# Kernel optimization log

Hardware: AMD Instinct MI355X
Metric: run time of the kernel (lower is better)

Reference implementation:

```python
import jax, jax.numpy as jnp
import numpy as np

B, H, W, C = 16, 64, 64, 512
NH, WS, SS = 16, 8, 4
HD = C // NH
N = WS * WS
MLP = 4 * C
EPS = 1e-5


def window_partition(x, ws):
    b, h, w, c = x.shape
    x = x.reshape(b, h // ws, ws, w // ws, ws, c).transpose(0, 1, 3, 2, 4, 5)
    return x.reshape(-1, ws, ws, c)


def window_reverse(win, ws, h, w):
    c = win.shape[-1]
    x = win.reshape(-1, h // ws, w // ws, ws, ws, c).transpose(0, 1, 3, 2, 4, 5)
    return x.reshape(-1, h, w, c)


def _rel_pos_index():
    coords = np.stack(np.meshgrid(np.arange(WS), np.arange(WS), indexing='ij'))  # [2,WS,WS]
    cf = coords.reshape(2, -1)
    rc = (cf[:, :, None] - cf[:, None, :]).transpose(1, 2, 0)  # [N,N,2]
    rc[:, :, 0] += WS - 1
    rc[:, :, 1] += WS - 1
    rc[:, :, 0] *= 2 * WS - 1
    return jnp.asarray(rc.sum(-1), dtype=jnp.int32)  # [N,N]


def _attn_mask():
    # region ids for shifted windows (HF get_attn_mask)
    img = np.zeros((1, H, W, 1), dtype=np.float32)
    slices = (slice(0, -WS), slice(-WS, -SS), slice(-SS, None))
    cnt = 0
    for hs in slices:
        for ws_ in slices:
            img[:, hs, ws_, :] = cnt
            cnt += 1
    mw = np.asarray(window_partition(jnp.asarray(img), WS)).reshape(-1, N)  # [nw,N]
    mask = mw[:, None, :] - mw[:, :, None]
    mask = np.where(mask != 0, -100.0, 0.0).astype(np.float32)
    return jnp.asarray(mask)  # [nw,N,N]


REL_IDX = _rel_pos_index()
ATTN_MASK = _attn_mask()


def layer_norm(x, g, b):
    mu = x.mean(-1, keepdims=True)
    var = ((x - mu) ** 2).mean(-1, keepdims=True)
    return (x - mu) * jax.lax.rsqrt(var + EPS) * g + b


def setup_inputs() -> dict:
    key = jax.random.key(0)
    ks = jax.random.split(key, 16)
    s = 0.02
    return {
        'hidden_states': jax.random.normal(ks[0], (B, H * W, C), jnp.float32),
        'q_w': jax.random.normal(ks[1], (C, C), jnp.float32) * s,
        'q_b': jnp.zeros((C,), jnp.float32),
        'k_w': jax.random.normal(ks[2], (C, C), jnp.float32) * s,
        'k_b': jnp.zeros((C,), jnp.float32),
        'v_w': jax.random.normal(ks[3], (C, C), jnp.float32) * s,
        'v_b': jnp.zeros((C,), jnp.float32),
        'proj_w': jax.random.normal(ks[4], (C, C), jnp.float32) * s,
        'proj_b': jnp.zeros((C,), jnp.float32),
        'rel_bias_table': jax.random.normal(ks[5], ((2 * WS - 1) * (2 * WS - 1), NH), jnp.float32) * s,
        'ln1_w': jnp.ones((C,), jnp.float32),
        'ln1_b': jnp.zeros((C,), jnp.float32),
        'ln2_w': jnp.ones((C,), jnp.float32),
        'ln2_b': jnp.zeros((C,), jnp.float32),
        'fc1_w': jax.random.normal(ks[6], (MLP, C), jnp.float32) * s,
        'fc1_b': jnp.zeros((MLP,), jnp.float32),
        'fc2_w': jax.random.normal(ks[7], (C, MLP), jnp.float32) * s,
        'fc2_b': jnp.zeros((C,), jnp.float32),
    }


def reference(hidden_states, q_w, q_b, k_w, k_b, v_w, v_b, proj_w, proj_b,
              rel_bias_table, ln1_w, ln1_b, ln2_w, ln2_b, fc1_w, fc1_b, fc2_w, fc2_b):
    shortcut = hidden_states
    x = layer_norm(hidden_states, ln1_w, ln1_b).reshape(B, H, W, C)
    # cyclic shift
    x = jnp.roll(x, (-SS, -SS), axis=(1, 2))
    win = window_partition(x, WS).reshape(-1, N, C)  # [B*nw, N, C]
    Bw = win.shape[0]

    def heads(t):  # [Bw,N,C] -> [Bw,NH,N,HD]
        return t.reshape(Bw, N, NH, HD).transpose(0, 2, 1, 3)

    q = heads(win @ q_w.T + q_b)
    k = heads(win @ k_w.T + k_b)
    v = heads(win @ v_w.T + v_b)

    scores = jnp.einsum('bhnd,bhmd->bhnm', q, k) / jnp.sqrt(jnp.float32(HD))
    bias = rel_bias_table[REL_IDX.reshape(-1)].reshape(N, N, NH).transpose(2, 0, 1)  # [NH,N,N]
    scores = scores + bias[None]
    nw = ATTN_MASK.shape[0]
    scores = scores.reshape(Bw // nw, nw, NH, N, N) + ATTN_MASK[None, :, None]
    scores = scores.reshape(Bw, NH, N, N)
    probs = jax.nn.softmax(scores, axis=-1)
    ctx = jnp.einsum('bhnm,bhmd->bhnd', probs, v).transpose(0, 2, 1, 3).reshape(Bw, N, C)
    attn_out = ctx @ proj_w.T + proj_b

    shifted = window_reverse(attn_out.reshape(-1, WS, WS, C), WS, H, W)
    x = jnp.roll(shifted, (SS, SS), axis=(1, 2)).reshape(B, H * W, C)
    h = shortcut + x

    y = layer_norm(h, ln2_w, ln2_b)
    y = jax.nn.gelu(y @ fc1_w.T + fc1_b, approximate=False)
    y = y @ fc2_w.T + fc2_b
    return h + y
```

## Files before the change

kernel.cpp:

```cpp
#include <hip/hip_runtime.h>
#include <cmath>
#include <cstdint>
#include <cstddef>

typedef __bf16 bf16;
typedef __bf16 bf16x8 __attribute__((ext_vector_type(8)));
typedef float f32x4 __attribute__((ext_vector_type(4)));

#define DEVINL __device__ __forceinline__

DEVINL void gload_lds16(const bf16* g, bf16* l) {
    __builtin_amdgcn_global_load_lds(
        (const __attribute__((address_space(1))) void*)g,
        (__attribute__((address_space(3))) void*)l,
        16, 0, 0);
}

DEVINL bool probe_f32(const uint32_t* probe) { return *probe == 0x3F800000u; }

#define OFF_QW  0u
#define OFF_KW  262144u
#define OFF_VW  524288u
#define OFF_PW  786432u
#define OFF_F1W 1048576u
#define OFF_F2W 2097152u
#define OFF_REL 3145728u
#define OFF_QB  3149328u
#define OFF_KB  3149840u
#define OFF_VB  3150352u
#define OFF_PB  3150864u
#define OFF_L1W 3151376u
#define OFF_L1B 3151888u
#define OFF_L2W 3152400u
#define OFF_L2B 3152912u
#define OFF_F1B 3153424u
#define OFF_F2B 3155472u
#define PRM_TOT 3155984u

struct P17 { const void* p[17]; };

__global__ __launch_bounds__(256) void conv_params(P17 ps, const uint32_t* probe,
                                                   bf16* __restrict__ dst) {
    const size_t off[18] = {OFF_QW, OFF_KW, OFF_VW, OFF_PW, OFF_F1W, OFF_F2W,
                            OFF_REL, OFF_QB, OFF_KB, OFF_VB, OFF_PB, OFF_L1W,
                            OFF_L1B, OFF_L2W, OFF_L2B, OFF_F1B, OFF_F2B, PRM_TOT};
    size_t e = ((size_t)blockIdx.x * 256 + threadIdx.x) * 8;
    if (e >= PRM_TOT) return;
    int s = 0;
#pragma unroll
    for (int i = 1; i < 17; ++i) s = (e >= off[i]) ? i : s;
    const size_t loc = e - off[s];
    if (probe_f32(probe)) {
        const float* sp = (const float*)ps.p[s] + loc;
        bf16x8 o;
#pragma unroll
        for (int t = 0; t < 8; ++t) o[t] = (bf16)sp[t];
        *(bf16x8*)(dst + e) = o;
    } else {
        *(bf16x8*)(dst + e) = *(const bf16x8*)((const bf16*)ps.p[s] + loc);
    }
}

__global__ __launch_bounds__(256) void conv_hidden(const void* __restrict__ src,
                                                   const uint32_t* probe,
                                                   bf16* __restrict__ dst,
                                                   size_t base_elt) {
    size_t e = ((size_t)blockIdx.x * 256 + threadIdx.x) * 8;
    if (probe_f32(probe)) {
        const float* sp = (const float*)src + base_elt + e;
        bf16x8 o;
#pragma unroll
        for (int t = 0; t < 8; ++t) o[t] = (bf16)sp[t];
        *(bf16x8*)(dst + e) = o;
    } else {
        *(bf16x8*)(dst + e) = *(const bf16x8*)((const bf16*)src + base_elt + e);
    }
}

template <int MODE>
__global__ __launch_bounds__(256) void ln_kernel(const bf16* __restrict__ srcb,
                                                 const float* __restrict__ srcf,
                                                 const bf16* __restrict__ g,
                                                 const bf16* __restrict__ bb,
                                                 bf16* __restrict__ out) {
    const int row = blockIdx.x * 4 + (threadIdx.x >> 6);
    const int lane = threadIdx.x & 63;
    size_t srow;
    if (MODE == 0) {
        int win = row >> 6, t = row & 63;
        int b = win >> 6, wi = win & 63;
        int hs = ((wi >> 3) << 3) + (t >> 3);
        int ws = ((wi & 7) << 3) + (t & 7);
        srow = (size_t)b * 4096 + (size_t)((hs + 4) & 63) * 64 + ((ws + 4) & 63);
    } else {
        srow = row;
    }
    float x[8];
    if (MODE == 0) {
        bf16x8 vv = *(const bf16x8*)(srcb + srow * 512 + lane * 8);
#pragma unroll
        for (int t = 0; t < 8; ++t) x[t] = (float)vv[t];
    } else {
        const f32x4* p = (const f32x4*)(srcf + srow * 512 + lane * 8);
        f32x4 a = p[0], c = p[1];
#pragma unroll
        for (int t = 0; t < 4; ++t) { x[t] = a[t]; x[4 + t] = c[t]; }
    }
    float s = 0.f, s2 = 0.f;
#pragma unroll
    for (int t = 0; t < 8; ++t) { s += x[t]; s2 += x[t] * x[t]; }
    for (int off = 1; off < 64; off <<= 1) {
        s += __shfl_xor(s, off, 64);
        s2 += __shfl_xor(s2, off, 64);
    }
    const float mu = s * (1.0f / 512.0f);
    const float var = s2 * (1.0f / 512.0f) - mu * mu;
    const float rs = rsqrtf(var + 1e-5f);
    bf16x8 gg = *(const bf16x8*)(g + lane * 8);
    bf16x8 bv = *(const bf16x8*)(bb + lane * 8);
    bf16x8 o;
#pragma unroll
    for (int t = 0; t < 8; ++t)
        o[t] = (bf16)(((x[t] - mu) * rs) * (float)gg[t] + (float)bv[t]);
    *(bf16x8*)(out + (size_t)row * 512 + lane * 8) = o;
}

template <int N, int K, int EPI>
__global__ __launch_bounds__(256) void gemm_bt(const bf16* __restrict__ A,
                                               const bf16* __restrict__ W,
                                               const bf16* __restrict__ bias,
                                               void* __restrict__ outp,
                                               const bf16* __restrict__ auxb,
                                               const float* __restrict__ auxf,
                                               size_t obase,
                                               const uint32_t* probe) {
    __shared__ bf16 sA[128 * 32];
    __shared__ bf16 sB[128 * 32];
    const int tid = threadIdx.x;
    const int bm = blockIdx.x, bn = blockIdx.y;
    const int wave = tid >> 6, lane = tid & 63;
    const int wm = (wave >> 1) << 6, wn = (wave & 1) << 6;
    const int lrow = lane & 15, quad = lane >> 4;

    bool f32o = false;
    if constexpr (EPI == 3) f32o = probe_f32(probe);

    f32x4 acc[4][4] = {};
    const bf16* Ab = A + (size_t)bm * 128 * K;
    const bf16* Wb = W + (size_t)bn * 128 * K;

    const int e0 = tid * 8;
    const int e1 = (256 + tid) * 8;
    const int r0 = e0 >> 5, c0 = e0 & 31;
    const int r1 = e1 >> 5, c1 = e1 & 31;

    for (int k0 = 0; k0 < K; k0 += 32) {
        gload_lds16(Ab + (size_t)r0 * K + k0 + c0, &sA[e0]);
        gload_lds16(Ab + (size_t)r1 * K + k0 + c1, &sA[e1]);
        gload_lds16(Wb + (size_t)r0 * K + k0 + c0, &sB[e0]);
        gload_lds16(Wb + (size_t)r1 * K + k0 + c1, &sB[e1]);
        __syncthreads();
        bf16x8 af[4], bfr[4];
#pragma unroll
        for (int i = 0; i < 4; ++i)
            af[i] = *(const bf16x8*)&sA[(wm + i * 16 + lrow) * 32 + quad * 8];
#pragma unroll
        for (int j = 0; j < 4; ++j)
            bfr[j] = *(const bf16x8*)&sB[(wn + j * 16 + lrow) * 32 + quad * 8];
#pragma unroll
        for (int i = 0; i < 4; ++i)
#pragma unroll
            for (int j = 0; j < 4; ++j)
                acc[i][j] = __builtin_amdgcn_mfma_f32_16x16x32_bf16(af[i], bfr[j], acc[i][j], 0, 0, 0);
        __syncthreads();
    }

#pragma unroll
    for (int i = 0; i < 4; ++i) {
#pragma unroll
        for (int r = 0; r < 4; ++r) {
            const int m = bm * 128 + wm + i * 16 + quad * 4 + r;
            size_t dest = 0;
            if (EPI == 1) {
                int win = m >> 6, t = m & 63;
                int b = win >> 6, wi = win & 63;
                int hs = ((wi >> 3) << 3) + (t >> 3);
                int ws = ((wi & 7) << 3) + (t & 7);
                dest = (size_t)b * 4096 + (size_t)((hs + 4) & 63) * 64 + ((ws + 4) & 63);
            }
#pragma unroll
            for (int j = 0; j < 4; ++j) {
                const int n = bn * 128 + wn + j * 16 + lrow;
                float v = acc[i][j][r] + (float)bias[n];
                if (EPI == 0) {
                    ((bf16*)outp)[(size_t)m * N + n] = (bf16)v;
                } else if (EPI == 1) {
                    ((float*)outp)[dest * 512 + n] = v + (float)auxb[dest * 512 + n];
                } else if (EPI == 2) {
                    float gl = 0.5f * v * (1.0f + erff(v * 0.70710678118654752f));
                    ((bf16*)outp)[(size_t)m * N + n] = (bf16)gl;
                } else {
                    float o = v + auxf[(size_t)m * N + n];
                    if (f32o) ((float*)outp)[obase + (size_t)m * N + n] = o;
                    else      ((bf16*)outp)[obase + (size_t)m * N + n] = (bf16)o;
                }
            }
        }
    }
}

__global__ __launch_bounds__(256) void attn_kernel(const bf16* __restrict__ q,
                                                   const bf16* __restrict__ k,
                                                   const bf16* __restrict__ v,
                                                   const bf16* __restrict__ table,
                                                   bf16* __restrict__ ctx) {
    __shared__ bf16 sVt[4][32 * 64];
    __shared__ bf16 sP[4][64 * 64];
    const int win = blockIdx.x;
    const int wave = threadIdx.x >> 6, lane = threadIdx.x & 63;
    const int head = blockIdx.y * 4 + wave;
    const int lrow = lane & 15, quad = lane >> 4;
    const size_t base = (size_t)win * 64 * 512 + head * 32;

    {
        const bf16* vr = v + base + (size_t)lane * 512;
#pragma unroll
        for (int d0 = 0; d0 < 32; d0 += 8) {
            bf16x8 vv = *(const bf16x8*)(vr + d0);
#pragma unroll
            for (int t = 0; t < 8; ++t) sVt[wave][(d0 + t) * 64 + lane] = vv[t];
        }
    }

    f32x4 sacc[4][4] = {};
    {
        bf16x8 qa[4], kb[4];
#pragma unroll
        for (int i = 0; i < 4; ++i)
            qa[i] = *(const bf16x8*)(q + base + (size_t)(i * 16 + lrow) * 512 + quad * 8);
#pragma unroll
        for (int j = 0; j < 4; ++j)
            kb[j] = *(const bf16x8*)(k + base + (size_t)(j * 16 + lrow) * 512 + quad * 8);
#pragma unroll
        for (int i = 0; i < 4; ++i)
#pragma unroll
            for (int j = 0; j < 4; ++j)
                sacc[i][j] = __builtin_amdgcn_mfma_f32_16x16x32_bf16(qa[i], kb[j], sacc[i][j], 0, 0, 0);
    }

    const int wi = win & 63;
    const int hb8 = (wi >> 3) << 3, wb8 = (wi & 7) << 3;
    const float scale = 0.17677669529663689f;
#pragma unroll
    for (int ti = 0; ti < 4; ++ti) {
#pragma unroll
        for (int r = 0; r < 4; ++r) {
            const int i = ti * 16 + quad * 4 + r;
            const int ih = i >> 3, iw = i & 7;
            const int ah = hb8 + ih, aw = wb8 + iw;
            const int rgi = ((ah < 56) ? 0 : (ah < 60) ? 1 : 2) * 3 +
                            ((aw < 56) ? 0 : (aw < 60) ? 1 : 2);
            float rowmax = -1e30f;
#pragma unroll
            for (int tj = 0; tj < 4; ++tj) {
                const int j = tj * 16 + lrow;
                const int jh = j >> 3, jw = j & 7;
                const int bh = hb8 + jh, bw = wb8 + jw;
                const int rgj = ((bh < 56) ? 0 : (bh < 60) ? 1 : 2) * 3 +
                                ((bw < 56) ? 0 : (bw < 60) ? 1 : 2);
                const int ridx = (ih - jh + 7) * 15 + (iw - jw + 7);
                float sv = sacc[ti][tj][r] * scale + (float)table[ridx * 16 + head] +
                           ((rgi == rgj) ? 0.0f : -100.0f);
                sacc[ti][tj][r] = sv;
                rowmax = fmaxf(rowmax, sv);
            }
            for (int off = 1; off < 16; off <<= 1)
                rowmax = fmaxf(rowmax, __shfl_xor(rowmax, off, 64));
            float rsum = 0.f;
#pragma unroll
            for (int tj = 0; tj < 4; ++tj) {
                float e = __expf(sacc[ti][tj][r] - rowmax);
                sacc[ti][tj][r] = e;
                rsum += e;
            }
            for (int off = 1; off < 16; off <<= 1) rsum += __shfl_xor(rsum, off, 64);
            const float inv = 1.0f / rsum;
#pragma unroll
            for (int tj = 0; tj < 4; ++tj)
                sP[wave][(size_t)i * 64 + tj * 16 + lrow] = (bf16)(sacc[ti][tj][r] * inv);
        }
    }
    __syncthreads();

    f32x4 cacc[4][2] = {};
#pragma unroll
    for (int ks = 0; ks < 2; ++ks) {
        bf16x8 vbf[2];
#pragma unroll
        for (int tn = 0; tn < 2; ++tn)
            vbf[tn] = *(const bf16x8*)&sVt[wave][(tn * 16 + lrow) * 64 + ks * 32 + quad * 8];
#pragma unroll
        for (int mi = 0; mi < 4; ++mi) {
            bf16x8 pa = *(const bf16x8*)&sP[wave][(size_t)(mi * 16 + lrow) * 64 + ks * 32 + quad * 8];
#pragma unroll
            for (int tn = 0; tn < 2; ++tn)
                cacc[mi][tn] = __builtin_amdgcn_mfma_f32_16x16x32_bf16(pa, vbf[tn], cacc[mi][tn], 0, 0, 0);
        }
    }
#pragma unroll
    for (int mi = 0; mi < 4; ++mi)
#pragma unroll
        for (int tn = 0; tn < 2; ++tn)
#pragma unroll
            for (int r = 0; r < 4; ++r) {
                const int i = mi * 16 + quad * 4 + r;
                const int d = tn * 16 + lrow;
                ctx[base + (size_t)i * 512 + d] = (bf16)cacc[mi][tn][r];
            }
}

extern "C" void kernel_launch(void* const* d_in, const int* in_sizes, int n_in,
                              void* d_out, int out_size, void* d_ws, size_t ws_size,
                              hipStream_t stream) {
    (void)in_sizes; (void)n_in; (void)out_size;
    const uint32_t* probe = (const uint32_t*)d_in[10];
    char* ws = (char*)d_ws;
    const size_t MB = (size_t)1 << 20;

    bf16* prm = (bf16*)ws;
    P17 ps;
    ps.p[0] = d_in[1];  ps.p[1] = d_in[3];  ps.p[2] = d_in[5];  ps.p[3] = d_in[7];
    ps.p[4] = d_in[14]; ps.p[5] = d_in[16]; ps.p[6] = d_in[9];  ps.p[7] = d_in[2];
    ps.p[8] = d_in[4];  ps.p[9] = d_in[6];  ps.p[10] = d_in[8]; ps.p[11] = d_in[10];
    ps.p[12] = d_in[11]; ps.p[13] = d_in[12]; ps.p[14] = d_in[13];
    ps.p[15] = d_in[15]; ps.p[16] = d_in[17];
    conv_params<<<dim3((PRM_TOT / 8 + 255) / 256), dim3(256), 0, stream>>>(ps, probe, prm);

    int nb = 1;
    for (int c = 16; c >= 2; c >>= 1)
        if (8 * MB + (size_t)c * 36 * MB <= ws_size) { nb = c; break; }
    const size_t R = (size_t)nb * 4096;
    char* arena = ws + 8 * MB;
    bf16* hidC = (bf16*)(arena);
    bf16* Xc   = (bf16*)(arena + 1024 * R);
    bf16* qc   = (bf16*)(arena + 2048 * R);
    bf16* kc   = (bf16*)(arena + 3072 * R);
    bf16* vc   = (bf16*)(arena + 4096 * R);
    float* hc  = (float*)(arena + 5120 * R);
    bf16* a1   = (bf16*)(arena + 7168 * R);

    const int nchunks = 16 / nb;
    const size_t Mh = R / 2;

    for (int cb = 0; cb < nchunks; ++cb) {
        conv_hidden<<<dim3((unsigned)(R / 4)), dim3(256), 0, stream>>>(
            d_in[0], probe, hidC, (size_t)cb * R * 512);

        ln_kernel<0><<<dim3((unsigned)(R / 4)), dim3(256), 0, stream>>>(
            hidC, nullptr, prm + OFF_L1W, prm + OFF_L1B, Xc);

        gemm_bt<512, 512, 0><<<dim3((unsigned)(R / 128), 4), dim3(256), 0, stream>>>(
            Xc, prm + OFF_QW, prm + OFF_QB, qc, nullptr, nullptr, 0, nullptr);
        gemm_bt<512, 512, 0><<<dim3((unsigned)(R / 128), 4), dim3(256), 0, stream>>>(
            Xc, prm + OFF_KW, prm + OFF_KB, kc, nullptr, nullptr, 0, nullptr);
        gemm_bt<512, 512, 0><<<dim3((unsigned)(R / 128), 4), dim3(256), 0, stream>>>(
            Xc, prm + OFF_VW, prm + OFF_VB, vc, nullptr, nullptr, 0, nullptr);

        attn_kernel<<<dim3((unsigned)(R / 64), 4), dim3(256), 0, stream>>>(
            qc, kc, vc, prm + OFF_REL, Xc);

        gemm_bt<512, 512, 1><<<dim3((unsigned)(R / 128), 4), dim3(256), 0, stream>>>(
            Xc, prm + OFF_PW, prm + OFF_PB, hc, hidC, nullptr, 0, nullptr);

        ln_kernel<1><<<dim3((unsigned)(R / 4)), dim3(256), 0, stream>>>(
            nullptr, hc, prm + OFF_L2W, prm + OFF_L2B, Xc);

        for (int hf = 0; hf < 2; ++hf) {
            gemm_bt<2048, 512, 2><<<dim3((unsigned)(Mh / 128), 16), dim3(256), 0, stream>>>(
                Xc + (size_t)hf * Mh * 512, prm + OFF_F1W, prm + OFF_F1B, a1,
                nullptr, nullptr, 0, nullptr);
            gemm_bt<512, 2048, 3><<<dim3((unsigned)(Mh / 128), 4), dim3(256), 0, stream>>>(
                a1, prm + OFF_F2W, prm + OFF_F2B, d_out,
                nullptr, hc + (size_t)hf * Mh * 512,
                ((size_t)cb * R + (size_t)hf * Mh) * 512, probe);
        }
    }
}
```

Baseline: 1.271 ms.

## Rewrite GEMM as 256x256-tile, 8-wave, double-buffered swizzled LDS pipeline

Result: slower. 1.978 ms (+55.7%).

```diff
diff --git a/kernel.cpp b/kernel.cpp
--- a/kernel.cpp
+++ b/kernel.cpp
@@ -125,8 +125,115 @@
     *(bf16x8*)(out + (size_t)row * 512 + lane * 8) = o;
 }
 
+
+template <int K>
+DEVINL void stage_two(const bf16* src, char* reg, int k0, int tid, int sswz,
+                      int X0, int X1) {
+    {
+        const int X = X0 + tid * 16;
+        const int sx = X ^ sswz;
+        gload_lds16(src + (size_t)(sx >> 7) * K + (k0 + ((sx & 127) >> 1)),
+                    (bf16*)(reg + X));
+    }
+    {
+        const int X = X1 + tid * 16;
+        const int sx = X ^ sswz;
+        gload_lds16(src + (size_t)(sx >> 7) * K + (k0 + ((sx & 127) >> 1)),
+                    (bf16*)(reg + X));
+    }
+}
+
+template <int K, int PART>
+DEVINL void stage_part(const bf16* Ab, const bf16* Wb, char* lds, int tile,
+                       int tid, int sswz) {
+    constexpr bool isB = (PART == 1 || PART == 3);
+    constexpr int X0 = (PART == 0) ? 0 : (PART == 1) ? 0 : (PART == 2) ? 8192 : 16384;
+    constexpr int X1 = (PART == 0) ? 16384 : (PART == 1) ? 8192 : 24576;
+    char* reg = lds + (tile & 1) * 65536 + (isB ? 32768 : 0);
+    stage_two<K>(isB ? Wb : Ab, reg, tile * 64, tid, sswz, X0, X1);
+}
+
+DEVINL bf16x8 lds_frag(const char* base, int row, int cb, int rswz) {
+    return *(const bf16x8*)(base + ((row * 128 + cb) ^ rswz));
+}
+
+template <int IOFF, int JLO>
+DEVINL void mfma_quad(bf16x8 (&Ar)[4][2], bf16x8 (&Br)[4][2], f32x4 (&acc)[8][4]) {
+#pragma unroll
+    for (int i = 0; i < 4; ++i)
+#pragma unroll
+        for (int j = 0; j < 2; ++j)
+#pragma unroll
+            for (int ks = 0; ks < 2; ++ks)
+                acc[i + IOFF][j + JLO] = __builtin_amdgcn_mfma_f32_16x16x32_bf16(
+                    Ar[i][ks], Br[j + JLO][ks], acc[i + IOFF][j + JLO], 0, 0, 0);
+}
+
+DEVINL void phase_open() {
+    __builtin_amdgcn_s_barrier();
+    __builtin_amdgcn_sched_barrier(0);
+    __builtin_amdgcn_s_setprio(1);
+}
+DEVINL void phase_close() {
+    __builtin_amdgcn_s_setprio(0);
+    __builtin_amdgcn_sched_barrier(0);
+    __builtin_amdgcn_s_barrier();
+}
+
+template <int K, bool S1, bool S2, int VM>
+DEVINL void ktile(const bf16* Ab, const bf16* Wb, char* lds, int t, int tid,
+                  int wm, int wn, int lrow, int quad, int rswz, int sswz,
+                  f32x4 (&acc)[8][4]) {
+    const char* aA = lds + (t & 1) * 65536;
+    const char* aB = aA + 32768;
+    const int cb = quad * 16;
+    bf16x8 Ar[4][2], Br[4][2];
+#pragma unroll
+    for (int i = 0; i < 4; ++i) {
+        Ar[i][0] = lds_frag(aA, wm + i * 16 + lrow, cb, rswz);
+        Ar[i][1] = lds_frag(aA, wm + i * 16 + lrow, cb + 64, rswz);
+    }
+#pragma unroll
+    for (int j = 0; j < 2; ++j) {
+        Br[j][0] = lds_frag(aB, wn + j * 16 + lrow, cb, rswz);
+        Br[j][1] = lds_frag(aB, wn + j * 16 + lrow, cb + 64, rswz);
+    }
+    if constexpr (S1) stage_part<K, 3>(Ab, Wb, lds, t + 1, tid, sswz);
+    phase_open();
+    mfma_quad<0, 0>(Ar, Br, acc);
+    phase_close();
+#pragma unroll
+    for (int j = 2; j < 4; ++j) {
+        Br[j][0] = lds_frag(aB, wn + j * 16 + lrow, cb, rswz);
+        Br[j][1] = lds_frag(aB, wn + j * 16 + lrow, cb + 64, rswz);
+    }
+    if constexpr (S2) stage_part<K, 0>(Ab, Wb, lds, t + 2, tid, sswz);
+    phase_open();
+    mfma_quad<0, 2>(Ar, Br, acc);
+    phase_close();
+#pragma unroll
+    for (int i = 0; i < 4; ++i) {
+        Ar[i][0] = lds_frag(aA, wm + 64 + i * 16 + lrow, cb, rswz);
+        Ar[i][1] = lds_frag(aA, wm + 64 + i * 16 + lrow, cb + 64, rswz);
+    }
+    if constexpr (S2) stage_part<K, 1>(Ab, Wb, lds, t + 2, tid, sswz);
+    phase_open();
+    mfma_quad<4, 0>(Ar, Br, acc);
+    phase_close();
+    if constexpr (S2) stage_part<K, 2>(Ab, Wb, lds, t + 2, tid, sswz);
+    __builtin_amdgcn_s_barrier();
+    __builtin_amdgcn_sched_barrier(0);
+    __builtin_amdgcn_s_setprio(1);
+    mfma_quad<4, 2>(Ar, Br, acc);
+    __builtin_amdgcn_s_setprio(0);
+    __builtin_amdgcn_sched_barrier(0);
+    if constexpr (VM == 6) asm volatile("s_waitcnt vmcnt(6)" ::: "memory");
+    if constexpr (VM == 0) asm volatile("s_waitcnt vmcnt(0)" ::: "memory");
+    __builtin_amdgcn_s_barrier();
+}
+
 template <int N, int K, int EPI>
-__global__ __launch_bounds__(256) void gemm_bt(const bf16* __restrict__ A,
+__global__ __launch_bounds__(512) void gemm_bt(const bf16* __restrict__ A,
                                                const bf16* __restrict__ W,
                                                const bf16* __restrict__ bias,
                                                void* __restrict__ outp,
@@ -134,52 +241,47 @@
                                                const float* __restrict__ auxf,
                                                size_t obase,
                                                const uint32_t* probe) {
-    __shared__ bf16 sA[128 * 32];
-    __shared__ bf16 sB[128 * 32];
+    static_assert(K % 64 == 0 && K / 64 >= 2, "K must be multiple of 64, >=128");
+    extern __shared__ char lds[];
     const int tid = threadIdx.x;
     const int bm = blockIdx.x, bn = blockIdx.y;
     const int wave = tid >> 6, lane = tid & 63;
-    const int wm = (wave >> 1) << 6, wn = (wave & 1) << 6;
+    const int wm = (wave >> 2) << 7;
+    const int wn = (wave & 3) << 6;
     const int lrow = lane & 15, quad = lane >> 4;
+    const int rswz = (lrow & 4) << 3;
+    const int sswz = lane & 32;
+
+    const bf16* Ab = A + (size_t)bm * 256 * K;
+    const bf16* Wb = W + (size_t)bn * 256 * K;
+
+    f32x4 acc[8][4] = {};
+
+    stage_part<K, 0>(Ab, Wb, lds, 0, tid, sswz);
+    stage_part<K, 1>(Ab, Wb, lds, 0, tid, sswz);
+    stage_part<K, 2>(Ab, Wb, lds, 0, tid, sswz);
+    stage_part<K, 3>(Ab, Wb, lds, 0, tid, sswz);
+    stage_part<K, 0>(Ab, Wb, lds, 1, tid, sswz);
+    stage_part<K, 1>(Ab, Wb, lds, 1, tid, sswz);
+    stage_part<K, 2>(Ab, Wb, lds, 1, tid, sswz);
+    asm volatile("s_waitcnt vmcnt(6)" ::: "memory");
+    __builtin_amdgcn_s_barrier();
+
+    constexpr int NT = K / 64;
+#pragma unroll 2
+    for (int t = 0; t < NT - 2; ++t)
+        ktile<K, true, true, 6>(Ab, Wb, lds, t, tid, wm, wn, lrow, quad, rswz, sswz, acc);
+    ktile<K, true, false, 0>(Ab, Wb, lds, NT - 2, tid, wm, wn, lrow, quad, rswz, sswz, acc);
+    ktile<K, false, false, -1>(Ab, Wb, lds, NT - 1, tid, wm, wn, lrow, quad, rswz, sswz, acc);
 
     bool f32o = false;
     if constexpr (EPI == 3) f32o = probe_f32(probe);
 
-    f32x4 acc[4][4] = {};
-    const bf16* Ab = A + (size_t)bm * 128 * K;
-    const bf16* Wb = W + (size_t)bn * 128 * K;
-
-    const int e0 = tid * 8;
-    const int e1 = (256 + tid) * 8;
-    const int r0 = e0 >> 5, c0 = e0 & 31;
-    const int r1 = e1 >> 5, c1 = e1 & 31;
-
-    for (int k0 = 0; k0 < K; k0 += 32) {
-        gload_lds16(Ab + (size_t)r0 * K + k0 + c0, &sA[e0]);
-        gload_lds16(Ab + (size_t)r1 * K + k0 + c1, &sA[e1]);
-        gload_lds16(Wb + (size_t)r0 * K + k0 + c0, &sB[e0]);
-        gload_lds16(Wb + (size_t)r1 * K + k0 + c1, &sB[e1]);
-        __syncthreads();
-        bf16x8 af[4], bfr[4];
-#pragma unroll
-        for (int i = 0; i < 4; ++i)
-            af[i] = *(const bf16x8*)&sA[(wm + i * 16 + lrow) * 32 + quad * 8];
-#pragma unroll
-        for (int j = 0; j < 4; ++j)
-            bfr[j] = *(const bf16x8*)&sB[(wn + j * 16 + lrow) * 32 + quad * 8];
-#pragma unroll
-        for (int i = 0; i < 4; ++i)
-#pragma unroll
-            for (int j = 0; j < 4; ++j)
-                acc[i][j] = __builtin_amdgcn_mfma_f32_16x16x32_bf16(af[i], bfr[j], acc[i][j], 0, 0, 0);
-        __syncthreads();
-    }
-
-#pragma unroll
-    for (int i = 0; i < 4; ++i) {
+#pragma unroll
+    for (int i = 0; i < 8; ++i) {
 #pragma unroll
         for (int r = 0; r < 4; ++r) {
-            const int m = bm * 128 + wm + i * 16 + quad * 4 + r;
+            const int m = bm * 256 + wm + i * 16 + quad * 4 + r;
             size_t dest = 0;
             if (EPI == 1) {
                 int win = m >> 6, t = m & 63;
@@ -190,7 +292,7 @@
             }
 #pragma unroll
             for (int j = 0; j < 4; ++j) {
-                const int n = bn * 128 + wn + j * 16 + lrow;
+                const int n = bn * 256 + wn + j * 16 + lrow;
                 float v = acc[i][j][r] + (float)bias[n];
                 if (EPI == 0) {
                     ((bf16*)outp)[(size_t)m * N + n] = (bf16)v;
@@ -323,6 +425,20 @@
                               void* d_out, int out_size, void* d_ws, size_t ws_size,
                               hipStream_t stream) {
     (void)in_sizes; (void)n_in; (void)out_size;
+
+    static bool attr_set = false;
+    if (!attr_set) {
+        attr_set = true;
+        (void)hipFuncSetAttribute(reinterpret_cast<const void*>(&gemm_bt<512, 512, 0>),
+                                  hipFuncAttributeMaxDynamicSharedMemorySize, 131072);
+        (void)hipFuncSetAttribute(reinterpret_cast<const void*>(&gemm_bt<512, 512, 1>),
+                                  hipFuncAttributeMaxDynamicSharedMemorySize, 131072);
+        (void)hipFuncSetAttribute(reinterpret_cast<const void*>(&gemm_bt<2048, 512, 2>),
+                                  hipFuncAttributeMaxDynamicSharedMemorySize, 131072);
+        (void)hipFuncSetAttribute(reinterpret_cast<const void*>(&gemm_bt<512, 2048, 3>),
+                                  hipFuncAttributeMaxDynamicSharedMemorySize, 131072);
+    }
+
     const uint32_t* probe = (const uint32_t*)d_in[10];
     char* ws = (char*)d_ws;
     const size_t MB = (size_t)1 << 20;
@@ -359,27 +475,27 @@
         ln_kernel<0><<<dim3((unsigned)(R / 4)), dim3(256), 0, stream>>>(
             hidC, nullptr, prm + OFF_L1W, prm + OFF_L1B, Xc);
 
-        gemm_bt<512, 512, 0><<<dim3((unsigned)(R / 128), 4), dim3(256), 0, stream>>>(
+        gemm_bt<512, 512, 0><<<dim3((unsigned)(R / 256), 2), dim3(512), 131072, stream>>>(
             Xc, prm + OFF_QW, prm + OFF_QB, qc, nullptr, nullptr, 0, nullptr);
-        gemm_bt<512, 512, 0><<<dim3((unsigned)(R / 128), 4), dim3(256), 0, stream>>>(
+        gemm_bt<512, 512, 0><<<dim3((unsigned)(R / 256), 2), dim3(512), 131072, stream>>>(
             Xc, prm + OFF_KW, prm + OFF_KB, kc, nullptr, nullptr, 0, nullptr);
-        gemm_bt<512, 512, 0><<<dim3((unsigned)(R / 128), 4), dim3(256), 0, stream>>>(
+        gemm_bt<512, 512, 0><<<dim3((unsigned)(R / 256), 2), dim3(512), 131072, stream>>>(
             Xc, prm + OFF_VW, prm + OFF_VB, vc, nullptr, nullptr, 0, nullptr);
 
         attn_kernel<<<dim3((unsigned)(R / 64), 4), dim3(256), 0, stream>>>(
             qc, kc, vc, prm + OFF_REL, Xc);
 
-        gemm_bt<512, 512, 1><<<dim3((unsigned)(R / 128), 4), dim3(256), 0, stream>>>(
+        gemm_bt<512, 512, 1><<<dim3((unsigned)(R / 256), 2), dim3(512), 131072, stream>>>(
             Xc, prm + OFF_PW, prm + OFF_PB, hc, hidC, nullptr, 0, nullptr);
 
         ln_kernel<1><<<dim3((unsigned)(R / 4)), dim3(256), 0, stream>>>(
             nullptr, hc, prm + OFF_L2W, prm + OFF_L2B, Xc);
 
         for (int hf = 0; hf < 2; ++hf) {
-            gemm_bt<2048, 512, 2><<<dim3((unsigned)(Mh / 128), 16), dim3(256), 0, stream>>>(
+            gemm_bt<2048, 512, 2><<<dim3((unsigned)(Mh / 256), 8), dim3(512), 131072, stream>>>(
                 Xc + (size_t)hf * Mh * 512, prm + OFF_F1W, prm + OFF_F1B, a1,
                 nullptr, nullptr, 0, nullptr);
-            gemm_bt<512, 2048, 3><<<dim3((unsigned)(Mh / 128), 4), dim3(256), 0, stream>>>(
+            gemm_bt<512, 2048, 3><<<dim3((unsigned)(Mh / 256), 2), dim3(512), 131072, stream>>>(
                 a1, prm + OFF_F2W, prm + OFF_F2B, d_out,
                 nullptr, hc + (size_t)hf * Mh * 512,
                 ((size_t)cb * R + (size_t)hf * Mh) * 512, probe);
```

## Double GEMM K-tile to 64 and XOR-swizzle LDS layout

Applied to the files above, without the earlier changes.

Result: faster. 1.222 ms (-3.8%).

```diff
diff --git a/kernel.cpp b/kernel.cpp
--- a/kernel.cpp
+++ b/kernel.cpp
@@ -134,14 +134,22 @@
                                                const float* __restrict__ auxf,
                                                size_t obase,
                                                const uint32_t* probe) {
-    __shared__ bf16 sA[128 * 32];
-    __shared__ bf16 sB[128 * 32];
+    static_assert(K % 64 == 0, "K must be a multiple of 64");
+    __shared__ __align__(16) char sA[16384];
+    __shared__ __align__(16) char sB[16384];
     const int tid = threadIdx.x;
     const int bm = blockIdx.x, bn = blockIdx.y;
     const int wave = tid >> 6, lane = tid & 63;
     const int wm = (wave >> 1) << 6, wn = (wave & 1) << 6;
     const int lrow = lane & 15, quad = lane >> 4;
 
+    const uint32_t rsw = (uint32_t)(lrow & 7) << 4;
+    const uint32_t cb0 = ((uint32_t)(quad * 16)) ^ rsw;
+    const uint32_t cb1 = ((uint32_t)(quad * 16 + 64)) ^ rsw;
+    const int sswz = (tid & 56) << 1;
+    const uint32_t arow = (uint32_t)(wm + lrow) * 128u;
+    const uint32_t brow = (uint32_t)(wn + lrow) * 128u;
+
     bool f32o = false;
     if constexpr (EPI == 3) f32o = probe_f32(probe);
 
@@ -149,29 +157,32 @@
     const bf16* Ab = A + (size_t)bm * 128 * K;
     const bf16* Wb = W + (size_t)bn * 128 * K;
 
-    const int e0 = tid * 8;
-    const int e1 = (256 + tid) * 8;
-    const int r0 = e0 >> 5, c0 = e0 & 31;
-    const int r1 = e1 >> 5, c1 = e1 & 31;
-
-    for (int k0 = 0; k0 < K; k0 += 32) {
-        gload_lds16(Ab + (size_t)r0 * K + k0 + c0, &sA[e0]);
-        gload_lds16(Ab + (size_t)r1 * K + k0 + c1, &sA[e1]);
-        gload_lds16(Wb + (size_t)r0 * K + k0 + c0, &sB[e0]);
-        gload_lds16(Wb + (size_t)r1 * K + k0 + c1, &sB[e1]);
+    for (int k0 = 0; k0 < K; k0 += 64) {
+#pragma unroll
+        for (int r = 0; r < 4; ++r) {
+            const int X = r * 4096 + tid * 16;
+            const int sx = X ^ sswz;
+            const int row = sx >> 7, col = (sx & 127) >> 1;
+            gload_lds16(Ab + (size_t)row * K + k0 + col, (bf16*)(sA + X));
+            gload_lds16(Wb + (size_t)row * K + k0 + col, (bf16*)(sB + X));
+        }
         __syncthreads();
-        bf16x8 af[4], bfr[4];
+        bf16x8 af[4][2], bfr[4][2];
+#pragma unroll
+        for (int i = 0; i < 4; ++i) {
+            af[i][0]  = *(const bf16x8*)(sA + (arow + i * 2048 + cb0));
+            af[i][1]  = *(const bf16x8*)(sA + (arow + i * 2048 + cb1));
+            bfr[i][0] = *(const bf16x8*)(sB + (brow + i * 2048 + cb0));
+            bfr[i][1] = *(const bf16x8*)(sB + (brow + i * 2048 + cb1));
+        }
 #pragma unroll
         for (int i = 0; i < 4; ++i)
-            af[i] = *(const bf16x8*)&sA[(wm + i * 16 + lrow) * 32 + quad * 8];
-#pragma unroll
-        for (int j = 0; j < 4; ++j)
-            bfr[j] = *(const bf16x8*)&sB[(wn + j * 16 + lrow) * 32 + quad * 8];
-#pragma unroll
-        for (int i = 0; i < 4; ++i)
 #pragma unroll
             for (int j = 0; j < 4; ++j)
-                acc[i][j] = __builtin_amdgcn_mfma_f32_16x16x32_bf16(af[i], bfr[j], acc[i][j], 0, 0, 0);
+#pragma unroll
+                for (int ks = 0; ks < 2; ++ks)
+                    acc[i][j] = __builtin_amdgcn_mfma_f32_16x16x32_bf16(
+                        af[i][ks], bfr[j][ks], acc[i][j], 0, 0, 0);
         __syncthreads();
     }
 
```
